# Performance work log

Measured on AMD Instinct MI355X. Metric: run time of the kernel, lower is better.

Reference implementation:

```python
import jax, jax.numpy as jnp
import numpy as np

ALPHA = 1.0
BETA = 1.0
N_TDA = 16      # n: points subsampled per diagram
Q = 2.0         # Wasserstein order
NN_SIZE = 5     # knn size (self + 4 neighbors)
RADIUS = 0.07
H = 0.03
EPS = 1e-12
B, N = 8, 4096


def _sqdist(a, b):
    # a: [..., M, 3], b: [..., K, 3] -> [..., M, K] squared Euclidean distances
    aa = jnp.sum(a * a, -1)[..., :, None]
    bb = jnp.sum(b * b, -1)[..., None, :]
    ab = jnp.einsum('...md,...kd->...mk', a, b)
    return aa + bb - 2.0 * ab


def _mst_deaths(pts):
    # H0 persistence of Vietoris-Rips complex: births all 0, finite deaths are
    # the edge weights of the MST of the complete graph (Prim's algorithm).
    n = pts.shape[0]
    d = jnp.sqrt(jnp.maximum(_sqdist(pts, pts), 0.0))  # [n, n]
    in_tree = jnp.zeros((n,), bool).at[0].set(True)
    mind = d[0]  # distance from each node to the current tree

    def step(carry, _):
        in_tree, mind = carry
        m = jnp.where(in_tree, jnp.inf, mind)
        j = jnp.argmin(m)
        w = m[j]
        in_tree = in_tree.at[j].set(True)
        mind = jnp.minimum(mind, d[j])
        return (in_tree, mind), w

    _, deaths = jax.lax.scan(step, (in_tree, mind), None, length=n - 1)
    return deaths  # [n-1]


def _forward(pred, gt, pcd_radius):
    b = pred.shape[0]
    # ---- EMD loss (nearest-neighbor surrogate of CUDA auction_match) ----
    cost = _sqdist(pred, gt)                              # [B, N, N]
    idx = jnp.argmin(cost, axis=-1)                       # [B, N]
    matched = jnp.take_along_axis(gt, idx[..., None], axis=1)
    d2 = jnp.mean(((pred - matched) ** 2).reshape(b, -1), axis=1, keepdims=True)
    emd = jnp.mean(d2 / pcd_radius)
    # ---- Repulsion loss ----
    dpp = _sqdist(pred, pred)                             # [B, N, N]
    _, knn = jax.lax.top_k(-dpp, NN_SIZE)                 # nearest incl. self
    knn = knn[:, :, 1:]                                   # drop self -> [B, N, 4]
    grouped = jax.vmap(lambda p, ix: p[ix])(pred, knn)    # [B, N, 4, 3]
    r2 = jnp.maximum(jnp.sum((grouped - pred[:, :, None, :]) ** 2, -1), EPS)
    dist = jnp.sqrt(r2)
    rep = jnp.mean((RADIUS - dist) * jnp.exp(-r2 / H ** 2))
    # ---- TDA loss (per-sample VR H0 diagram + q-Wasserstein) ----
    key = jax.random.key(42)
    kp, kg = jax.random.split(key)

    def sub(k, pts):
        ix = jax.random.permutation(k, pts.shape[0])[:N_TDA]
        return pts[ix]

    pred_s = jax.vmap(sub)(jax.random.split(kp, b), pred)  # [B, 16, 3]
    gt_s = jax.vmap(sub)(jax.random.split(kg, b), gt)
    dp = jnp.sort(jax.vmap(_mst_deaths)(pred_s), axis=-1)  # [B, 15]
    dg = jnp.sort(jax.vmap(_mst_deaths)(gt_s), axis=-1)
    wd = jnp.sum(jnp.abs(dp - dg) ** Q, axis=-1) ** (1.0 / Q)
    tda = jnp.mean(wd)
    return (emd * 100.0, rep * ALPHA, tda * BETA)


def setup_inputs() -> dict:
    key = jax.random.key(0)
    k1, k2, k3 = jax.random.split(key, 3)
    pred = jax.random.normal(k1, (B, N, 3), jnp.float32)
    gt = jax.random.normal(k2, (B, N, 3), jnp.float32)
    pcd_radius = jax.random.uniform(k3, (B, 1), jnp.float32) + 0.5
    return {"pred": pred, "gt": gt, "pcd_radius": pcd_radius}


def reference(pred, gt, pcd_radius):
    return _forward(pred, gt, pcd_radius)
```

## Files before the change

kernel.cpp:

```cpp
#include <hip/hip_runtime.h>
#include <cstdint>
#include <cmath>
#include <vector>
#include <algorithm>
#include <numeric>

#define B_SZ 8
#define N_PTS 4096
#define NSPLIT 32
#define JTILE (N_PTS / NSPLIT)
#define RCUT2 0.10f

struct TdaArgs { int idx[16][16]; };

#define WS_BT(p)   ((float*)(p))
#define WS_KNN(p)  ((unsigned short*)((char*)(p) + 0x400000))
#define WS_PART(p) ((double*)((char*)(p) + 0xF00000))

__global__ __launch_bounds__(256, 4)
void emd_kernel(const float* __restrict__ pred, const float* __restrict__ gt,
                float* __restrict__ bt_out) {
  __shared__ float4 sg[JTILE];
  const int tid = threadIdx.x;
  const int xb  = blockIdx.x;
  const int b   = blockIdx.y;
  const int q   = blockIdx.z;
  const int jbase = q * JTILE;

  const float* src = gt + ((size_t)b * N_PTS + jbase) * 3;
  if (tid < JTILE) {
    float x = src[3 * tid + 0], y = src[3 * tid + 1], z = src[3 * tid + 2];
    sg[tid] = make_float4(x, y, z, -0.5f * fmaf(x, x, fmaf(y, y, z * z)));
  }

  const float* pb = pred + (size_t)b * N_PTS * 3;
  const int ibase = xb * 2048 + tid;
  float px[8], py[8], pz[8], bt[8];
  #pragma unroll
  for (int ii = 0; ii < 8; ++ii) {
    int i = ibase + ii * 256;
    px[ii] = pb[3 * i + 0]; py[ii] = pb[3 * i + 1]; pz[ii] = pb[3 * i + 2];
    bt[ii] = -INFINITY;
  }
  __syncthreads();

  for (int j0 = 0; j0 < JTILE; j0 += 8) {
    float4 g[8];
    #pragma unroll
    for (int k = 0; k < 8; ++k) g[k] = sg[j0 + k];
    #pragma unroll
    for (int ii = 0; ii < 8; ++ii) {
      #pragma unroll
      for (int k = 0; k < 8; ++k) {
        float t = fmaf(px[ii], g[k].x, fmaf(py[ii], g[k].y, fmaf(pz[ii], g[k].z, g[k].w)));
        bt[ii] = fmaxf(bt[ii], t);
      }
    }
  }
  #pragma unroll
  for (int ii = 0; ii < 8; ++ii)
    bt_out[((size_t)q * B_SZ + b) * N_PTS + ibase + ii * 256] = bt[ii];
}

__global__ __launch_bounds__(256, 4)
void rep_kernel(const float* __restrict__ pred, unsigned short* __restrict__ knn_out) {
  __shared__ float4 sg[JTILE];
  const int tid = threadIdx.x;
  const int xb  = blockIdx.x;
  const int b   = blockIdx.y;
  const int q   = blockIdx.z;
  const int jbase = q * JTILE;

  const float* pb = pred + (size_t)b * N_PTS * 3;
  const float* src = pb + (size_t)jbase * 3;
  if (tid < JTILE) {
    float x = src[3 * tid + 0], y = src[3 * tid + 1], z = src[3 * tid + 2];
    sg[tid] = make_float4(x, y, z, -0.5f * fmaf(x, x, fmaf(y, y, z * z)));
  }

  const int ibase = xb * 1024 + tid;
  float px[4], py[4], pz[4];
  float t0[4], t1[4], t2[4], t3[4], t4[4];
  int   i0v[4], i1v[4], i2v[4], i3v[4], i4v[4];
  #pragma unroll
  for (int ii = 0; ii < 4; ++ii) {
    int i = ibase + ii * 256;
    px[ii] = pb[3 * i + 0]; py[ii] = pb[3 * i + 1]; pz[ii] = pb[3 * i + 2];
    float pn = fmaf(px[ii], px[ii], fmaf(py[ii], py[ii], pz[ii] * pz[ii]));
    float tcut = 0.5f * (pn - RCUT2);
    t0[ii] = tcut; t1[ii] = tcut; t2[ii] = tcut; t3[ii] = tcut; t4[ii] = tcut;
    i0v[ii] = 0xFFFF; i1v[ii] = 0xFFFF; i2v[ii] = 0xFFFF; i3v[ii] = 0xFFFF; i4v[ii] = 0xFFFF;
  }
  __syncthreads();

  #define INS(ii, tt, jj) { \
    t4[ii] = tt; i4v[ii] = jj; \
    if (t4[ii] > t3[ii]) { float f = t3[ii]; t3[ii] = t4[ii]; t4[ii] = f; int p_ = i3v[ii]; i3v[ii] = i4v[ii]; i4v[ii] = p_; } \
    if (t3[ii] > t2[ii]) { float f = t2[ii]; t2[ii] = t3[ii]; t3[ii] = f; int p_ = i2v[ii]; i2v[ii] = i3v[ii]; i3v[ii] = p_; } \
    if (t2[ii] > t1[ii]) { float f = t1[ii]; t1[ii] = t2[ii]; t2[ii] = f; int p_ = i1v[ii]; i1v[ii] = i2v[ii]; i2v[ii] = p_; } \
    if (t1[ii] > t0[ii]) { float f = t0[ii]; t0[ii] = t1[ii]; t1[ii] = f; int p_ = i0v[ii]; i0v[ii] = i1v[ii]; i1v[ii] = p_; } }
  for (int j0 = 0; j0 < JTILE; j0 += 8) {
    float4 g[8];
    #pragma unroll
    for (int k = 0; k < 8; ++k) g[k] = sg[j0 + k];
    #pragma unroll
    for (int ii = 0; ii < 4; ++ii) {
      #pragma unroll
      for (int k = 0; k < 8; ++k) {
        float t = fmaf(px[ii], g[k].x, fmaf(py[ii], g[k].y, fmaf(pz[ii], g[k].z, g[k].w)));
        if (t > t4[ii]) INS(ii, t, j0 + k);
      }
    }
  }
  #undef INS

  #pragma unroll
  for (int ii = 0; ii < 4; ++ii) {
    size_t base = (((size_t)q * B_SZ + b) * N_PTS + ibase + ii * 256) * 5;
    knn_out[base + 0] = (i0v[ii] == 0xFFFF) ? 0xFFFF : (unsigned short)(jbase + i0v[ii]);
    knn_out[base + 1] = (i1v[ii] == 0xFFFF) ? 0xFFFF : (unsigned short)(jbase + i1v[ii]);
    knn_out[base + 2] = (i2v[ii] == 0xFFFF) ? 0xFFFF : (unsigned short)(jbase + i2v[ii]);
    knn_out[base + 3] = (i3v[ii] == 0xFFFF) ? 0xFFFF : (unsigned short)(jbase + i3v[ii]);
    knn_out[base + 4] = (i4v[ii] == 0xFFFF) ? 0xFFFF : (unsigned short)(jbase + i4v[ii]);
  }
}

__global__ __launch_bounds__(256)
void merge_kernel(const float* __restrict__ pred,
                  const float* __restrict__ bt_in, const unsigned short* __restrict__ knn_in,
                  double* __restrict__ partials) {
  __shared__ double wred[2][4];
  const int tid = threadIdx.x;
  const int blk = blockIdx.x;
  const int b   = blk >> 4;
  const int i   = (blk & 15) * 256 + tid;

  const float* pb = pred + (size_t)b * N_PTS * 3;
  const float px = pb[3 * i + 0], py = pb[3 * i + 1], pz = pb[3 * i + 2];
  const float pn = fmaf(px, px, fmaf(py, py, pz * pz));

  float bt = -INFINITY;
  for (int q = 0; q < NSPLIT; ++q)
    bt = fmaxf(bt, bt_in[((size_t)q * B_SZ + b) * N_PTS + i]);
  double emd = (double)fmaf(-2.0f, bt, pn);

  float s0 = INFINITY, s1 = INFINITY, s2 = INFINITY, s3 = INFINITY;
  int   j0v = 0x7fffffff, j1v = 0x7fffffff, j2v = 0x7fffffff, j3v = 0x7fffffff;
  for (int q = 0; q < NSPLIT; ++q) {
    const unsigned short* kn = knn_in + (((size_t)q * B_SZ + b) * N_PTS + i) * 5;
    #pragma unroll
    for (int c = 0; c < 5; ++c) {
      int v = kn[c];
      int idx = v & 0xFFF;
      float gx = pb[3 * idx + 0], gy = pb[3 * idx + 1], gz = pb[3 * idx + 2];
      float dx = px - gx, dy = py - gy, dz = pz - gz;
      float r2 = fmaf(dx, dx, fmaf(dy, dy, dz * dz));
      if (v >= 0xFFFF || idx == i) r2 = INFINITY;
      bool lt3 = (r2 < s3) || (r2 == s3 && idx < j3v);
      if (lt3) {
        s3 = r2; j3v = idx;
        if ((s3 < s2) || (s3 == s2 && j3v < j2v)) { float f = s2; s2 = s3; s3 = f; int p_ = j2v; j2v = j3v; j3v = p_; }
        if ((s2 < s1) || (s2 == s1 && j2v < j1v)) { float f = s1; s1 = s2; s2 = f; int p_ = j1v; j1v = j2v; j2v = p_; }
        if ((s1 < s0) || (s1 == s0 && j1v < j0v)) { float f = s0; s0 = s1; s1 = f; int p_ = j0v; j0v = j1v; j1v = p_; }
      }
    }
  }
  double rep = 0.0;
  {
    float rr[4] = { s0, s1, s2, s3 };
    #pragma unroll
    for (int k = 0; k < 4; ++k) {
      if (rr[k] < 1e30f) {
        float r2 = fmaxf(rr[k], 1e-12f);
        float dist = sqrtf(r2);
        rep += (double)((0.07f - dist) * expf(-r2 / 9.0e-4f));
      }
    }
  }

  double v0 = emd, v1 = rep;
  #pragma unroll
  for (int off = 32; off > 0; off >>= 1) { v0 += __shfl_down(v0, off); v1 += __shfl_down(v1, off); }
  if ((tid & 63) == 0) { wred[0][tid >> 6] = v0; wred[1][tid >> 6] = v1; }
  __syncthreads();
  if (tid == 0) {
    double a = 0.0, r = 0.0;
    #pragma unroll
    for (int w = 0; w < 4; ++w) { a += wred[0][w]; r += wred[1][w]; }
    partials[blk * 2 + 0] = a;
    partials[blk * 2 + 1] = r;
  }
}

__global__ __launch_bounds__(64)
void final_kernel(const float* __restrict__ pred, const float* __restrict__ gt,
                  const float* __restrict__ pcd, const double* __restrict__ partials,
                  float* __restrict__ out, TdaArgs args) {
  __shared__ float pts[16][16][3];
  __shared__ float aa[16][16];
  __shared__ float mind[16][16];
  __shared__ float deaths[16][15];
  __shared__ float wd[8];
  const int tid = threadIdx.x;

  if (tid < 16) {
    const float* src = (tid < 8) ? (pred + (size_t)tid * N_PTS * 3)
                                 : (gt + (size_t)(tid - 8) * N_PTS * 3);
    for (int k = 0; k < 16; ++k) {
      int ix = args.idx[tid][k];
      float x = src[3 * ix + 0], y = src[3 * ix + 1], z = src[3 * ix + 2];
      pts[tid][k][0] = x; pts[tid][k][1] = y; pts[tid][k][2] = z;
      aa[tid][k] = x * x + y * y + z * z;
    }
    #define DFORM(j, k) \
      sqrtf(fmaxf(aa[tid][j] + aa[tid][k] - 2.0f * (pts[tid][j][0] * pts[tid][k][0] + \
            pts[tid][j][1] * pts[tid][k][1] + pts[tid][j][2] * pts[tid][k][2]), 0.0f))
    for (int k = 0; k < 16; ++k) mind[tid][k] = DFORM(0, k);
    unsigned mask = 1u;
    for (int step = 0; step < 15; ++step) {
      float best = INFINITY; int bj = 0;
      for (int k = 0; k < 16; ++k) {
        float m = ((mask >> k) & 1u) ? INFINITY : mind[tid][k];
        if (m < best) { best = m; bj = k; }
      }
      deaths[tid][step] = best;
      mask |= (1u << bj);
      for (int k = 0; k < 16; ++k) mind[tid][k] = fminf(mind[tid][k], DFORM(bj, k));
    }
    #undef DFORM
    for (int a = 1; a < 15; ++a) {
      float v = deaths[tid][a];
      int c = a;
      while (c > 0 && deaths[tid][c - 1] > v) { deaths[tid][c] = deaths[tid][c - 1]; --c; }
      deaths[tid][c] = v;
    }
  }
  __syncthreads();
  if (tid < 8) {
    float s = 0.0f;
    for (int k = 0; k < 15; ++k) {
      float d = deaths[tid][k] - deaths[tid + 8][k];
      s += d * d;
    }
    wd[tid] = sqrtf(s);
  }
  __syncthreads();
  if (tid == 0) {
    double tda = 0.0;
    for (int b = 0; b < 8; ++b) tda += (double)wd[b];
    tda /= 8.0;
    double emd = 0.0;
    for (int b = 0; b < 8; ++b) {
      double s = 0.0;
      for (int c = 0; c < 16; ++c) s += partials[(b * 16 + c) * 2];
      emd += (s / (double)(N_PTS * 3)) / (double)pcd[b];
    }
    emd = emd / 8.0 * 100.0;
    double rep = 0.0;
    for (int k = 0; k < 128; ++k) rep += partials[k * 2 + 1];
    rep /= (double)(B_SZ * N_PTS * 4);
    out[0] = (float)emd;
    out[1] = (float)rep;
    out[2] = (float)tda;
  }
}

static inline uint32_t rotl32(uint32_t x, int d) { return (x << d) | (x >> (32 - d)); }

static void threefry2x32_host(uint32_t k0, uint32_t k1, uint32_t& x0, uint32_t& x1) {
  const uint32_t ks[3] = { k0, k1, k0 ^ k1 ^ 0x1BD11BDAu };
  static const int rot[2][4] = { {13, 15, 26, 6}, {17, 29, 16, 24} };
  x0 += ks[0]; x1 += ks[1];
  for (int i = 0; i < 5; ++i) {
    const int* r = rot[i & 1];
    for (int j = 0; j < 4; ++j) {
      x0 += x1;
      x1 = rotl32(x1, r[j]);
      x1 ^= x0;
    }
    x0 += ks[(i + 1) % 3];
    x1 += ks[(i + 2) % 3] + (uint32_t)(i + 1);
  }
}

static void jax_split_p(const uint32_t key[2], int n, uint32_t (*out)[2]) {
  for (int j = 0; j < n; ++j) {
    uint32_t a = 0u, b = (uint32_t)j;
    threefry2x32_host(key[0], key[1], a, b);
    out[j][0] = a; out[j][1] = b;
  }
}

static void jax_bits32_p(const uint32_t key[2], int n, uint32_t* bits) {
  for (int i = 0; i < n; ++i) {
    uint32_t a = 0u, b = (uint32_t)i;
    threefry2x32_host(key[0], key[1], a, b);
    bits[i] = a ^ b;
  }
}

static void jax_perm_first16(const uint32_t key_in[2], int n, int* out16) {
  std::vector<int> x((size_t)n);
  std::iota(x.begin(), x.end(), 0);
  uint32_t key[2] = { key_in[0], key_in[1] };
  const int rounds = (int)std::ceil(3.0 * std::log((double)n) / std::log(4294967295.0));
  std::vector<uint32_t> bits((size_t)n);
  std::vector<int> ord((size_t)n), nx((size_t)n);
  for (int r = 0; r < rounds; ++r) {
    uint32_t kr[2][2];
    jax_split_p(key, 2, kr);
    key[0] = kr[0][0]; key[1] = kr[0][1];
    jax_bits32_p(kr[1], n, bits.data());
    std::iota(ord.begin(), ord.end(), 0);
    std::stable_sort(ord.begin(), ord.end(),
                     [&](int A, int Bv) { return bits[A] < bits[Bv]; });
    for (int i = 0; i < n; ++i) nx[i] = x[ord[i]];
    x.swap(nx);
  }
  for (int i = 0; i < 16; ++i) out16[i] = x[i];
}

static void compute_tda_indices(TdaArgs& args) {
  const uint32_t root[2] = { 0u, 42u };
  uint32_t kpg[2][2];
  jax_split_p(root, 2, kpg);
  uint32_t kb[B_SZ][2];
  jax_split_p(kpg[0], B_SZ, kb);
  for (int b = 0; b < B_SZ; ++b) jax_perm_first16(kb[b], N_PTS, args.idx[b]);
  jax_split_p(kpg[1], B_SZ, kb);
  for (int b = 0; b < B_SZ; ++b) jax_perm_first16(kb[b], N_PTS, args.idx[8 + b]);
}


extern "C" void kernel_launch(void* const* d_in, const int* in_sizes, int n_in,
                              void* d_out, int out_size, void* d_ws, size_t ws_size,
                              hipStream_t stream) {
  const float* pred = (const float*)d_in[0];
  const float* gt   = (const float*)d_in[1];
  const float* pcd  = (const float*)d_in[2];
  float* out = (float*)d_out;

  TdaArgs targs;
  compute_tda_indices(targs);

  float*          bt   = WS_BT(d_ws);
  unsigned short* knn  = WS_KNN(d_ws);
  double*         part = WS_PART(d_ws);

  emd_kernel<<<dim3(2, B_SZ, NSPLIT), dim3(256), 0, stream>>>(pred, gt, bt);
  rep_kernel<<<dim3(4, B_SZ, NSPLIT), dim3(256), 0, stream>>>(pred, knn);
  merge_kernel<<<dim3(128), dim3(256), 0, stream>>>(pred, bt, knn, part);
  final_kernel<<<dim3(1), dim3(64), 0, stream>>>(pred, gt, pcd, part, out, targs);
}
```

Before: 4.767 ms.

## Split merge kernel's per-point split loop across four wavefronts and combine in LDS

Result: no change. 4.742 ms (-0.5%).

```diff
diff --git a/kernel.cpp b/kernel.cpp
--- a/kernel.cpp
+++ b/kernel.cpp
@@ -10,6 +10,7 @@
 #define NSPLIT 32
 #define JTILE (N_PTS / NSPLIT)
 #define RCUT2 0.10f
+#define MBLK 512
 
 struct TdaArgs { int idx[16][16]; };
 
@@ -125,28 +126,38 @@
   }
 }
 
-__global__ __launch_bounds__(256)
+#define LEXINS(r2, idx) { \
+  bool lt3 = (r2 < s3) || (r2 == s3 && idx < j3v); \
+  if (lt3) { \
+    s3 = r2; j3v = idx; \
+    if ((s3 < s2) || (s3 == s2 && j3v < j2v)) { float f = s2; s2 = s3; s3 = f; int p_ = j2v; j2v = j3v; j3v = p_; } \
+    if ((s2 < s1) || (s2 == s1 && j2v < j1v)) { float f = s1; s1 = s2; s2 = f; int p_ = j1v; j1v = j2v; j2v = p_; } \
+    if ((s1 < s0) || (s1 == s0 && j1v < j0v)) { float f = s0; s0 = s1; s1 = f; int p_ = j0v; j0v = j1v; j1v = p_; } \
+  } }
+
+__global__ __launch_bounds__(256, 2)
 void merge_kernel(const float* __restrict__ pred,
                   const float* __restrict__ bt_in, const unsigned short* __restrict__ knn_in,
                   double* __restrict__ partials) {
-  __shared__ double wred[2][4];
-  const int tid = threadIdx.x;
-  const int blk = blockIdx.x;
-  const int b   = blk >> 4;
-  const int i   = (blk & 15) * 256 + tid;
+  __shared__ float s_r2[4][64][5];
+  __shared__ int   s_ix[4][64][5];
+  __shared__ float s_bt[4][64];
+  const int tid  = threadIdx.x;
+  const int qg   = tid >> 6;
+  const int lane = tid & 63;
+  const int blk  = blockIdx.x;
+  const int b    = blk >> 6;
+  const int i    = (blk & 63) * 64 + lane;
 
   const float* pb = pred + (size_t)b * N_PTS * 3;
   const float px = pb[3 * i + 0], py = pb[3 * i + 1], pz = pb[3 * i + 2];
-  const float pn = fmaf(px, px, fmaf(py, py, pz * pz));
 
   float bt = -INFINITY;
-  for (int q = 0; q < NSPLIT; ++q)
-    bt = fmaxf(bt, bt_in[((size_t)q * B_SZ + b) * N_PTS + i]);
-  double emd = (double)fmaf(-2.0f, bt, pn);
-
   float s0 = INFINITY, s1 = INFINITY, s2 = INFINITY, s3 = INFINITY;
   int   j0v = 0x7fffffff, j1v = 0x7fffffff, j2v = 0x7fffffff, j3v = 0x7fffffff;
-  for (int q = 0; q < NSPLIT; ++q) {
+  const int q0 = qg * (NSPLIT / 4);
+  for (int q = q0; q < q0 + NSPLIT / 4; ++q) {
+    bt = fmaxf(bt, bt_in[((size_t)q * B_SZ + b) * N_PTS + i]);
     const unsigned short* kn = knn_in + (((size_t)q * B_SZ + b) * N_PTS + i) * 5;
     #pragma unroll
     for (int c = 0; c < 5; ++c) {
@@ -155,42 +166,50 @@
       float gx = pb[3 * idx + 0], gy = pb[3 * idx + 1], gz = pb[3 * idx + 2];
       float dx = px - gx, dy = py - gy, dz = pz - gz;
       float r2 = fmaf(dx, dx, fmaf(dy, dy, dz * dz));
-      if (v >= 0xFFFF || idx == i) r2 = INFINITY;
-      bool lt3 = (r2 < s3) || (r2 == s3 && idx < j3v);
-      if (lt3) {
-        s3 = r2; j3v = idx;
-        if ((s3 < s2) || (s3 == s2 && j3v < j2v)) { float f = s2; s2 = s3; s3 = f; int p_ = j2v; j2v = j3v; j3v = p_; }
-        if ((s2 < s1) || (s2 == s1 && j2v < j1v)) { float f = s1; s1 = s2; s2 = f; int p_ = j1v; j1v = j2v; j2v = p_; }
-        if ((s1 < s0) || (s1 == s0 && j1v < j0v)) { float f = s0; s0 = s1; s1 = f; int p_ = j0v; j0v = j1v; j1v = p_; }
-      }
-    }
-  }
-  double rep = 0.0;
-  {
-    float rr[4] = { s0, s1, s2, s3 };
-    #pragma unroll
-    for (int k = 0; k < 4; ++k) {
-      if (rr[k] < 1e30f) {
-        float r2 = fmaxf(rr[k], 1e-12f);
-        float dist = sqrtf(r2);
-        rep += (double)((0.07f - dist) * expf(-r2 / 9.0e-4f));
-      }
-    }
-  }
-
-  double v0 = emd, v1 = rep;
-  #pragma unroll
-  for (int off = 32; off > 0; off >>= 1) { v0 += __shfl_down(v0, off); v1 += __shfl_down(v1, off); }
-  if ((tid & 63) == 0) { wred[0][tid >> 6] = v0; wred[1][tid >> 6] = v1; }
-  __syncthreads();
-  if (tid == 0) {
-    double a = 0.0, r = 0.0;
-    #pragma unroll
-    for (int w = 0; w < 4; ++w) { a += wred[0][w]; r += wred[1][w]; }
-    partials[blk * 2 + 0] = a;
-    partials[blk * 2 + 1] = r;
-  }
-}
+      if (v >= 0xFFFF || idx == i) { r2 = INFINITY; idx = 0x7fffffff; }
+      LEXINS(r2, idx)
+    }
+  }
+  s_bt[qg][lane] = bt;
+  s_r2[qg][lane][0] = s0; s_r2[qg][lane][1] = s1; s_r2[qg][lane][2] = s2; s_r2[qg][lane][3] = s3;
+  s_ix[qg][lane][0] = j0v; s_ix[qg][lane][1] = j1v; s_ix[qg][lane][2] = j2v; s_ix[qg][lane][3] = j3v;
+  __syncthreads();
+
+  if (qg == 0) {
+    float s0 = INFINITY, s1 = INFINITY, s2 = INFINITY, s3 = INFINITY;
+    int   j0v = 0x7fffffff, j1v = 0x7fffffff, j2v = 0x7fffffff, j3v = 0x7fffffff;
+    float btall = -INFINITY;
+    #pragma unroll
+    for (int g = 0; g < 4; ++g) {
+      btall = fmaxf(btall, s_bt[g][lane]);
+      #pragma unroll
+      for (int k = 0; k < 4; ++k) {
+        float r2 = s_r2[g][lane][k];
+        int   idx = s_ix[g][lane][k];
+        LEXINS(r2, idx)
+      }
+    }
+    const float pn = fmaf(px, px, fmaf(py, py, pz * pz));
+    double emd = (double)fmaf(-2.0f, btall, pn);
+    double rep = 0.0;
+    {
+      float rr[4] = { s0, s1, s2, s3 };
+      #pragma unroll
+      for (int k = 0; k < 4; ++k) {
+        if (rr[k] < 1e30f) {
+          float r2 = fmaxf(rr[k], 1e-12f);
+          float dist = sqrtf(r2);
+          rep += (double)((0.07f - dist) * expf(-r2 / 9.0e-4f));
+        }
+      }
+    }
+    double v0 = emd, v1 = rep;
+    #pragma unroll
+    for (int off = 32; off > 0; off >>= 1) { v0 += __shfl_down(v0, off); v1 += __shfl_down(v1, off); }
+    if (lane == 0) { partials[blk * 2 + 0] = v0; partials[blk * 2 + 1] = v1; }
+  }
+}
+#undef LEXINS
 
 __global__ __launch_bounds__(64)
 void final_kernel(const float* __restrict__ pred, const float* __restrict__ gt,
@@ -201,6 +220,7 @@
   __shared__ float mind[16][16];
   __shared__ float deaths[16][15];
   __shared__ float wd[8];
+  __shared__ double emdb[8];
   const int tid = threadIdx.x;
 
   if (tid < 16) {
@@ -244,21 +264,25 @@
     }
     wd[tid] = sqrtf(s);
   }
+
+  double repsum = 0.0;
+  for (int k = tid; k < MBLK; k += 64) repsum += partials[k * 2 + 1];
+  #pragma unroll
+  for (int off = 32; off > 0; off >>= 1) repsum += __shfl_down(repsum, off);
+  if (tid < 8) {
+    double s = 0.0;
+    for (int c = 0; c < 64; ++c) s += partials[((tid << 6) + c) * 2];
+    emdb[tid] = (s / (double)(N_PTS * 3)) / (double)pcd[tid];
+  }
   __syncthreads();
   if (tid == 0) {
     double tda = 0.0;
     for (int b = 0; b < 8; ++b) tda += (double)wd[b];
     tda /= 8.0;
     double emd = 0.0;
-    for (int b = 0; b < 8; ++b) {
-      double s = 0.0;
-      for (int c = 0; c < 16; ++c) s += partials[(b * 16 + c) * 2];
-      emd += (s / (double)(N_PTS * 3)) / (double)pcd[b];
-    }
+    for (int b = 0; b < 8; ++b) emd += emdb[b];
     emd = emd / 8.0 * 100.0;
-    double rep = 0.0;
-    for (int k = 0; k < 128; ++k) rep += partials[k * 2 + 1];
-    rep /= (double)(B_SZ * N_PTS * 4);
+    double rep = repsum / (double)(B_SZ * N_PTS * 4);
     out[0] = (float)emd;
     out[1] = (float)rep;
     out[2] = (float)tda;
@@ -349,6 +373,6 @@
 
   emd_kernel<<<dim3(2, B_SZ, NSPLIT), dim3(256), 0, stream>>>(pred, gt, bt);
   rep_kernel<<<dim3(4, B_SZ, NSPLIT), dim3(256), 0, stream>>>(pred, knn);
-  merge_kernel<<<dim3(128), dim3(256), 0, stream>>>(pred, bt, knn, part);
+  merge_kernel<<<dim3(MBLK), dim3(256), 0, stream>>>(pred, bt, knn, part);
   final_kernel<<<dim3(1), dim3(64), 0, stream>>>(pred, gt, pcd, part, out, targs);
 }
```
